# Performance work log

Hardware: AMD Instinct MI355X
Metric: run time of the kernel (lower is better)

Reference implementation:

```python
import jax, jax.numpy as jnp
import numpy as np

N_NODES = 100000
NEG_SLOPE = 0.01  # F.leaky_relu default


def _hetero_graphconv(x, src, dst, W, b, n_nodes):
    """HeteroGraphConv(aggregate='sum') of DGL GraphConv(norm='both') per edge type.

    x: [N, d_in]; src/dst: [R, E] int; W: [R, d_in, d_out]; b: [R, d_out].
    """
    n_rel = W.shape[0]
    ones = None
    out = jnp.zeros((n_nodes, W.shape[2]), dtype=x.dtype)
    for r in range(n_rel):  # small fixed number of relations
        s, d = src[r], dst[r]
        e_ones = jnp.ones(s.shape, dtype=x.dtype)
        deg_out = jnp.clip(jax.ops.segment_sum(e_ones, s, num_segments=n_nodes), 1.0)
        deg_in = jnp.clip(jax.ops.segment_sum(e_ones, d, num_segments=n_nodes), 1.0)
        # norm='both': scale src by out_deg^-1/2, aggregate, scale dst by in_deg^-1/2.
        # Apply weight before gather (aggregation is linear) to shrink edge traffic.
        h = (x * (deg_out ** -0.5)[:, None]) @ W[r]          # [N, d_out]
        agg = jax.ops.segment_sum(h[s], d, num_segments=n_nodes)  # gather-scatter over edges
        out = out + agg * (deg_in ** -0.5)[:, None] + b[r]
    return out


def setup_inputs() -> dict:
    key = jax.random.key(0)
    ks = jax.random.split(key, 8)
    d_in, d_h, d_out, n_cls, n_rel, n_edges = 256, 128, 128, 16, 3, 600000
    x = jax.random.normal(ks[0], (N_NODES, d_in), dtype=jnp.float32)
    src = jax.random.randint(ks[1], (n_rel, n_edges), 0, N_NODES, dtype=jnp.int32)
    dst = jax.random.randint(ks[2], (n_rel, n_edges), 0, N_NODES, dtype=jnp.int32)
    W0 = jax.random.normal(ks[3], (n_rel, d_in, d_h), dtype=jnp.float32) * (d_in ** -0.5)
    b0 = jnp.zeros((n_rel, d_h), dtype=jnp.float32)
    W1 = jax.random.normal(ks[4], (n_rel, d_h, d_out), dtype=jnp.float32) * (d_h ** -0.5)
    b1 = jnp.zeros((n_rel, d_out), dtype=jnp.float32)
    fc_W = jax.random.normal(ks[5], (d_out, n_cls), dtype=jnp.float32) * (d_out ** -0.5)
    fc_b = jnp.zeros((n_cls,), dtype=jnp.float32)
    return {"x": x, "src": src, "dst": dst, "W0": W0, "b0": b0,
            "W1": W1, "b1": b1, "fc_W": fc_W, "fc_b": fc_b}


def reference(x, src, dst, W0, b0, W1, b1, fc_W, fc_b):
    n = x.shape[0]
    h = _hetero_graphconv(x, src, dst, W0, b0, n)
    h = jax.nn.leaky_relu(h, negative_slope=NEG_SLOPE)  # dropout rate 0 (eval)
    h = _hetero_graphconv(h, src, dst, W1, b1, n)       # last layer: no activation
    logits = h @ fc_W + fc_b
    return (h, logits)
```

## Files before the change

### kernel.cpp

```cpp
#include <hip/hip_runtime.h>
#include <hip/hip_bf16.h>
#include <stdint.h>


typedef __attribute__((ext_vector_type(8))) short bf16x8;
typedef __attribute__((ext_vector_type(4))) float f32x4;
typedef unsigned short u16;

#define CUR_PAD 16
#define BF_K 8
#define CAP 32

__global__ __launch_bounds__(256)
void gemm0_bucket(const float* __restrict__ A,
                  const u16* __restrict__ Whi_all, const u16* __restrict__ Wlo_all,
                  u16* __restrict__ Cout_all, int M, int K, int Nn,
                  const int* __restrict__ src, const int* __restrict__ dst,
                  int* __restrict__ cnt_out, int* __restrict__ cursor,
                  int* __restrict__ bkt, int E, int N) {
    __shared__ u16 As_hi[128][40];
    __shared__ u16 As_lo[128][40];
    __shared__ u16 Bs_hi[128][40];
    __shared__ u16 Bs_lo[128][40];

    const int role = blockIdx.x;

    if (role >= 3) {
        const int r = role - 3;
        const int nbk = (E + 256 * BF_K - 1) / (256 * BF_K);
        const int b = blockIdx.y;
        if (b >= nbk) return;
        int e0 = b * (256 * BF_K) + threadIdx.x;
        int s[BF_K], d[BF_K], pos[BF_K];
#pragma unroll
        for (int j = 0; j < BF_K; j++) {
            int e = e0 + j * 256;
            bool v = e < E;
            s[j] = v ? src[(size_t)r * E + e] : -1;
            d[j] = v ? dst[(size_t)r * E + e] : 0;
        }
#pragma unroll
        for (int j = 0; j < BF_K; j++)
            if (s[j] >= 0)
                atomicAdd(cnt_out + ((size_t)s[j] * 3 + r) * CUR_PAD, 1);
#pragma unroll
        for (int j = 0; j < BF_K; j++)
            pos[j] = (s[j] >= 0)
                   ? atomicAdd(cursor + ((size_t)d[j] * 3 + r) * CUR_PAD, 1) : 0;
#pragma unroll
        for (int j = 0; j < BF_K; j++)
            if (s[j] >= 0 && pos[j] < CAP)
                bkt[((size_t)d[j] * 3 + r) * CAP + pos[j]] = r * N + s[j];
        return;
    }

    const int r = role;
    const u16* Whi = Whi_all + (size_t)r * K * 128;
    const u16* Wlo = Wlo_all + (size_t)r * K * 128;
    u16* Cout = Cout_all + (size_t)r * Nn * 128;

    const int tid  = threadIdx.x;
    const int m0   = blockIdx.y * 128;
    const int lane = tid & 63;
    const int wave = tid >> 6;
    const int wm   = (wave & 1) * 64;
    const int wn   = (wave >> 1) * 64;
    const int lm   = lane & 15;
    const int kq   = (lane >> 4) * 8;

    f32x4 acc[4][4];
#pragma unroll
    for (int i = 0; i < 4; i++)
#pragma unroll
        for (int j = 0; j < 4; j++) acc[i][j] = (f32x4){0.f, 0.f, 0.f, 0.f};

    const int srow = tid >> 1;
    const int skb  = (tid & 1) * 16;

    const bool valid = (m0 + srow) < M;
    const float* arow = A + (size_t)(m0 + srow) * K;
    const u16* whrow = Whi + (size_t)srow * K;
    const u16* wlrow = Wlo + (size_t)srow * K;

    for (int k0 = 0; k0 < K; k0 += 32) {
        float fa[16];
        if (valid) {
            *(float4*)&fa[0]  = *(const float4*)(arow + k0 + skb);
            *(float4*)&fa[4]  = *(const float4*)(arow + k0 + skb + 4);
            *(float4*)&fa[8]  = *(const float4*)(arow + k0 + skb + 8);
            *(float4*)&fa[12] = *(const float4*)(arow + k0 + skb + 12);
        } else {
#pragma unroll
            for (int i = 0; i < 16; i++) fa[i] = 0.f;
        }
        uint32_t ah[8], al[8];
#pragma unroll
        for (int p = 0; p < 8; p++) {
            float f0 = fa[2 * p], f1 = fa[2 * p + 1];
            uint32_t u0 = __float_as_uint(f0), u1 = __float_as_uint(f1);
            ah[p] = (u0 >> 16) | (u1 & 0xFFFF0000u);
            float l0 = f0 - __uint_as_float(u0 & 0xFFFF0000u);
            float l1 = f1 - __uint_as_float(u1 & 0xFFFF0000u);
            al[p] = (__float_as_uint(l0) >> 16) | (__float_as_uint(l1) & 0xFFFF0000u);
        }
        *(uint4*)&As_hi[srow][skb]     = *(uint4*)&ah[0];
        *(uint4*)&As_hi[srow][skb + 8] = *(uint4*)&ah[4];
        *(uint4*)&As_lo[srow][skb]     = *(uint4*)&al[0];
        *(uint4*)&As_lo[srow][skb + 8] = *(uint4*)&al[4];

        *(uint4*)&Bs_hi[srow][skb]     = *(const uint4*)(whrow + k0 + skb);
        *(uint4*)&Bs_hi[srow][skb + 8] = *(const uint4*)(whrow + k0 + skb + 8);
        *(uint4*)&Bs_lo[srow][skb]     = *(const uint4*)(wlrow + k0 + skb);
        *(uint4*)&Bs_lo[srow][skb + 8] = *(const uint4*)(wlrow + k0 + skb + 8);

        __syncthreads();

        bf16x8 a_hi[4], a_lo[4], b_hi[4], b_lo[4];
#pragma unroll
        for (int i = 0; i < 4; i++) {
            a_hi[i] = *(const bf16x8*)&As_hi[wm + i * 16 + lm][kq];
            a_lo[i] = *(const bf16x8*)&As_lo[wm + i * 16 + lm][kq];
            b_hi[i] = *(const bf16x8*)&Bs_hi[wn + i * 16 + lm][kq];
            b_lo[i] = *(const bf16x8*)&Bs_lo[wn + i * 16 + lm][kq];
        }
#pragma unroll
        for (int i = 0; i < 4; i++)
#pragma unroll
            for (int j = 0; j < 4; j++) {
                acc[i][j] = __builtin_amdgcn_mfma_f32_16x16x32_bf16(a_hi[i], b_hi[j], acc[i][j], 0, 0, 0);
                acc[i][j] = __builtin_amdgcn_mfma_f32_16x16x32_bf16(a_lo[i], b_hi[j], acc[i][j], 0, 0, 0);
                acc[i][j] = __builtin_amdgcn_mfma_f32_16x16x32_bf16(a_hi[i], b_lo[j], acc[i][j], 0, 0, 0);
            }
        __syncthreads();
    }

    const int rq = (lane >> 4) * 4;
#pragma unroll
    for (int i = 0; i < 4; i++) {
        int mbase = m0 + wm + i * 16 + rq;
#pragma unroll
        for (int j = 0; j < 4; j++) {
            int col = wn + j * 16 + lm;
#pragma unroll
            for (int rg = 0; rg < 4; rg++) {
                int m = mbase + rg;
                if (m < M) {
                    uint32_t u = __float_as_uint(acc[i][j][rg]);
                    Cout[(size_t)m * 128 + col] =
                        (u16)((u + 0x7FFFu + ((u >> 16) & 1u)) >> 16);
                }
            }
        }
    }
}

__global__ __launch_bounds__(256)
void reduce_scales_kernel(const int* __restrict__ cnt_out, const int* __restrict__ cursor,
                          float* __restrict__ s_out, float* __restrict__ s_in, int N) {
    int n = blockIdx.x * blockDim.x + threadIdx.x;
    if (n >= N) return;
#pragma unroll
    for (int r = 0; r < 3; r++) {
        int co = cnt_out[((size_t)n * 3 + r) * CUR_PAD];
        s_out[(size_t)r * N + n] = rsqrtf(fmaxf((float)co, 1.0f));
        int ci = cursor[((size_t)n * 3 + r) * CUR_PAD];
        s_in[(size_t)r * N + n] = rsqrtf(fmaxf((float)ci, 1.0f));
    }
}

__global__ __launch_bounds__(256)
void prep_w_kernel(const float* __restrict__ W0, const float* __restrict__ W1,
                   u16* __restrict__ w0hi, u16* __restrict__ w0lo,
                   u16* __restrict__ w1hi, u16* __restrict__ w1lo) {
    int idx = blockIdx.x * blockDim.x + threadIdx.x;
    const int n0 = 3 * 256 * 128;
    const int n1 = 3 * 128 * 128;
    if (idx >= n0 + n1) return;
    float f;
    u16 *phi, *plo;
    int oidx;
    if (idx < n0) {
        int r = idx / 32768, rem = idx % 32768;
        int n = rem / 256, k = rem % 256;
        f = W0[(size_t)r * 32768 + (size_t)k * 128 + n];
        phi = w0hi; plo = w0lo; oidx = idx;
    } else {
        int i2 = idx - n0;
        int r = i2 / 16384, rem = i2 % 16384;
        int n = rem / 128, k = rem % 128;
        f = W1[(size_t)r * 16384 + (size_t)k * 128 + n];
        phi = w1hi; plo = w1lo; oidx = i2;
    }
    uint32_t u = __float_as_uint(f);
    phi[oidx] = (u16)(u >> 16);
    float lo = f - __uint_as_float(u & 0xFFFF0000u);
    uint32_t ul = __float_as_uint(lo);
    plo[oidx] = (u16)((ul + 0x7FFFu + ((ul >> 16) & 1u)) >> 16);
}

__global__ __launch_bounds__(256)
void gemm_split_bf16(const float* __restrict__ A, const float* __restrict__ s_out,
                     const u16* __restrict__ Whi_all, const u16* __restrict__ Wlo_all,
                     u16* __restrict__ Cout_all, int M, int K, int Nn) {
    const int r = blockIdx.y;
    const float* scale = s_out + (size_t)r * Nn;
    const u16* Whi = Whi_all + (size_t)r * K * 128;
    const u16* Wlo = Wlo_all + (size_t)r * K * 128;
    u16* Cout = Cout_all + (size_t)r * Nn * 128;

    __shared__ u16 As_hi[128][40];
    __shared__ u16 As_lo[128][40];
    __shared__ u16 Bs_hi[128][40];
    __shared__ u16 Bs_lo[128][40];

    const int tid  = threadIdx.x;
    const int m0   = blockIdx.x * 128;
    const int lane = tid & 63;
    const int wave = tid >> 6;
    const int wm   = (wave & 1) * 64;
    const int wn   = (wave >> 1) * 64;
    const int lm   = lane & 15;
    const int kq   = (lane >> 4) * 8;

    f32x4 acc[4][4];
#pragma unroll
    for (int i = 0; i < 4; i++)
#pragma unroll
        for (int j = 0; j < 4; j++) acc[i][j] = (f32x4){0.f, 0.f, 0.f, 0.f};

    const int srow = tid >> 1;
    const int skb  = (tid & 1) * 16;

    const bool valid = (m0 + srow) < M;
    const float sval = valid ? scale[m0 + srow] : 0.f;
    const float* arow = A + (size_t)(m0 + srow) * K;
    const u16* whrow = Whi + (size_t)srow * K;
    const u16* wlrow = Wlo + (size_t)srow * K;

    for (int k0 = 0; k0 < K; k0 += 32) {
        float fa[16];
        if (valid) {
            *(float4*)&fa[0]  = *(const float4*)(arow + k0 + skb);
            *(float4*)&fa[4]  = *(const float4*)(arow + k0 + skb + 4);
            *(float4*)&fa[8]  = *(const float4*)(arow + k0 + skb + 8);
            *(float4*)&fa[12] = *(const float4*)(arow + k0 + skb + 12);
        } else {
#pragma unroll
            for (int i = 0; i < 16; i++) fa[i] = 0.f;
        }
        uint32_t ah[8], al[8];
#pragma unroll
        for (int p = 0; p < 8; p++) {
            float f0 = fa[2 * p] * sval, f1 = fa[2 * p + 1] * sval;
            uint32_t u0 = __float_as_uint(f0), u1 = __float_as_uint(f1);
            ah[p] = (u0 >> 16) | (u1 & 0xFFFF0000u);
            float l0 = f0 - __uint_as_float(u0 & 0xFFFF0000u);
            float l1 = f1 - __uint_as_float(u1 & 0xFFFF0000u);
            al[p] = (__float_as_uint(l0) >> 16) | (__float_as_uint(l1) & 0xFFFF0000u);
        }
        *(uint4*)&As_hi[srow][skb]     = *(uint4*)&ah[0];
        *(uint4*)&As_hi[srow][skb + 8] = *(uint4*)&ah[4];
        *(uint4*)&As_lo[srow][skb]     = *(uint4*)&al[0];
        *(uint4*)&As_lo[srow][skb + 8] = *(uint4*)&al[4];

        *(uint4*)&Bs_hi[srow][skb]     = *(const uint4*)(whrow + k0 + skb);
        *(uint4*)&Bs_hi[srow][skb + 8] = *(const uint4*)(whrow + k0 + skb + 8);
        *(uint4*)&Bs_lo[srow][skb]     = *(const uint4*)(wlrow + k0 + skb);
        *(uint4*)&Bs_lo[srow][skb + 8] = *(const uint4*)(wlrow + k0 + skb + 8);

        __syncthreads();

        bf16x8 a_hi[4], a_lo[4], b_hi[4], b_lo[4];
#pragma unroll
        for (int i = 0; i < 4; i++) {
            a_hi[i] = *(const bf16x8*)&As_hi[wm + i * 16 + lm][kq];
            a_lo[i] = *(const bf16x8*)&As_lo[wm + i * 16 + lm][kq];
            b_hi[i] = *(const bf16x8*)&Bs_hi[wn + i * 16 + lm][kq];
            b_lo[i] = *(const bf16x8*)&Bs_lo[wn + i * 16 + lm][kq];
        }
#pragma unroll
        for (int i = 0; i < 4; i++)
#pragma unroll
            for (int j = 0; j < 4; j++) {
                acc[i][j] = __builtin_amdgcn_mfma_f32_16x16x32_bf16(a_hi[i], b_hi[j], acc[i][j], 0, 0, 0);
                acc[i][j] = __builtin_amdgcn_mfma_f32_16x16x32_bf16(a_lo[i], b_hi[j], acc[i][j], 0, 0, 0);
                acc[i][j] = __builtin_amdgcn_mfma_f32_16x16x32_bf16(a_hi[i], b_lo[j], acc[i][j], 0, 0, 0);
            }
        __syncthreads();
    }

    const int rq = (lane >> 4) * 4;
#pragma unroll
    for (int i = 0; i < 4; i++) {
        int mbase = m0 + wm + i * 16 + rq;
#pragma unroll
        for (int j = 0; j < 4; j++) {
            int col = wn + j * 16 + lm;
#pragma unroll
            for (int rg = 0; rg < 4; rg++) {
                int m = mbase + rg;
                if (m < M) {
                    uint32_t u = __float_as_uint(acc[i][j][rg]);
                    Cout[(size_t)m * 128 + col] =
                        (u16)((u + 0x7FFFu + ((u >> 16) & 1u)) >> 16);
                }
            }
        }
    }
}

#define BF16_LO(u) __uint_as_float((u) << 16)
#define BF16_HI(u) __uint_as_float((u) & 0xFFFF0000u)

template<bool SOUT>
__device__ __forceinline__ void gather_all(const uint32_t* __restrict__ hb32,
                                           const int* __restrict__ cursor,
                                           const int* __restrict__ bkt,
                                           const float* __restrict__ s_in,
                                           const float* __restrict__ s_out,
                                           int node, int lane, int N,
                                           float& ox, float& oy) {
    const uint32_t* hrow = hb32 + lane;
    int d0 = __builtin_amdgcn_readfirstlane(cursor[(size_t)node * (3 * CUR_PAD)]);
    int d1 = __builtin_amdgcn_readfirstlane(cursor[(size_t)node * (3 * CUR_PAD) + CUR_PAD]);
    int d2 = __builtin_amdgcn_readfirstlane(cursor[(size_t)node * (3 * CUR_PAD) + 2 * CUR_PAD]);
    d0 = d0 > CAP ? CAP : d0;
    d1 = d1 > CAP ? CAP : d1;
    d2 = d2 > CAP ? CAP : d2;
    const int t01 = d0 + d1;
    const int tot = t01 + d2;
    const int* bp = bkt + (size_t)node * (3 * CAP);
    const float w0 = s_in[node];
    const float w1 = s_in[(size_t)N + node];
    const float w2 = s_in[(size_t)2 * N + node];
    float ax = 0.f, ay = 0.f, bx = 0.f, by = 0.f;
    float cx = 0.f, cy = 0.f, dx = 0.f, dy = 0.f;
    for (int j = 0; j < tot; j += 8) {
        uint32_t u[8];
        float w[8];
#pragma unroll
        for (int p = 0; p < 8; p++) {
            int jj = j + p;
            int r2 = (jj >= d0 ? 1 : 0) + (jj >= t01 ? 1 : 0);
            int off = r2 == 0 ? 0 : (r2 == 1 ? d0 - CAP : t01 - 2 * CAP);
            int bval = bp[jj - off];
            bool act = jj < tot;
            int idx = act ? bval : 0;
            float ws = r2 == 0 ? w0 : (r2 == 1 ? w1 : w2);
            if (SOUT) ws *= s_out[idx];
            w[p] = act ? ws : 0.f;
            u[p] = hrow[(size_t)idx * 64];
        }
#pragma unroll
        for (int p = 0; p < 8; p += 4) {
            ax = fmaf(BF16_LO(u[p]),     w[p],     ax);
            ay = fmaf(BF16_HI(u[p]),     w[p],     ay);
            bx = fmaf(BF16_LO(u[p + 1]), w[p + 1], bx);
            by = fmaf(BF16_HI(u[p + 1]), w[p + 1], by);
            cx = fmaf(BF16_LO(u[p + 2]), w[p + 2], cx);
            cy = fmaf(BF16_HI(u[p + 2]), w[p + 2], cy);
            dx = fmaf(BF16_LO(u[p + 3]), w[p + 3], dx);
            dy = fmaf(BF16_HI(u[p + 3]), w[p + 3], dy);
        }
    }
    ox = (ax + bx) + (cx + dx);
    oy = (ay + by) + (cy + dy);
}

__global__ __launch_bounds__(256)
void gather_l0(const u16* __restrict__ hb, const int* __restrict__ cursor,
               const int* __restrict__ bkt, const float* __restrict__ s_in,
               const float* __restrict__ s_out,
               const float* __restrict__ b, float* __restrict__ out, int N) {
    int node = blockIdx.x * 4 + (threadIdx.x >> 6);
    if (node >= N) return;
    int lane = threadIdx.x & 63;
    float tx, ty;
    gather_all<true>((const uint32_t*)hb, cursor, bkt, s_in, s_out, node, lane, N, tx, ty);
    int c0 = lane * 2;
    tx += b[c0] + b[128 + c0] + b[256 + c0];
    ty += b[c0 + 1] + b[128 + c0 + 1] + b[256 + c0 + 1];
    tx = fmaxf(tx, 0.f) + 0.01f * fminf(tx, 0.f);
    ty = fmaxf(ty, 0.f) + 0.01f * fminf(ty, 0.f);
    *(float2*)(out + (size_t)node * 128 + c0) = make_float2(tx, ty);
}

__global__ __launch_bounds__(256)
void gather_l1(const u16* __restrict__ hb, const int* __restrict__ cursor,
               const int* __restrict__ bkt, const float* __restrict__ s_in,
               const float* __restrict__ b, const float* __restrict__ fcW,
               const float* __restrict__ fcb, float* __restrict__ out_h,
               float* __restrict__ out_logits, int N) {
    int node = blockIdx.x * 4 + (threadIdx.x >> 6);
    if (node >= N) return;
    int lane = threadIdx.x & 63;
    float tx, ty;
    gather_all<false>((const uint32_t*)hb, cursor, bkt, s_in, nullptr, node, lane, N, tx, ty);
    int c0 = lane * 2;
    tx += b[c0] + b[128 + c0] + b[256 + c0];
    ty += b[c0 + 1] + b[128 + c0 + 1] + b[256 + c0 + 1];
    *(float2*)(out_h + (size_t)node * 128 + c0) = make_float2(tx, ty);

    const float* fc0 = fcW + (size_t)c0 * 16;
    float p[16];
#pragma unroll
    for (int j = 0; j < 16; j++) p[j] = tx * fc0[j] + ty * fc0[16 + j];
#pragma unroll
    for (int off = 1; off < 64; off <<= 1) {
#pragma unroll
        for (int j = 0; j < 16; j++) p[j] += __shfl_xor(p[j], off);
    }
    if (lane == 0) {
        float* lp = out_logits + (size_t)node * 16;
        *(float4*)(lp + 0)  = make_float4(p[0] + fcb[0],  p[1] + fcb[1],  p[2] + fcb[2],  p[3] + fcb[3]);
        *(float4*)(lp + 4)  = make_float4(p[4] + fcb[4],  p[5] + fcb[5],  p[6] + fcb[6],  p[7] + fcb[7]);
        *(float4*)(lp + 8)  = make_float4(p[8] + fcb[8],  p[9] + fcb[9],  p[10] + fcb[10], p[11] + fcb[11]);
        *(float4*)(lp + 12) = make_float4(p[12] + fcb[12], p[13] + fcb[13], p[14] + fcb[14], p[15] + fcb[15]);
    }
}

extern "C" void kernel_launch(void* const* d_in, const int* in_sizes, int n_in,
                              void* d_out, int out_size, void* d_ws, size_t ws_size,
                              hipStream_t stream) {
    const float* x   = (const float*)d_in[0];
    const int*   src = (const int*)d_in[1];
    const int*   dst = (const int*)d_in[2];
    const float* W0  = (const float*)d_in[3];
    const float* b0  = (const float*)d_in[4];
    const float* W1  = (const float*)d_in[5];
    const float* b1  = (const float*)d_in[6];
    const float* fcW = (const float*)d_in[7];
    const float* fcb = (const float*)d_in[8];

    const int N = in_sizes[0] / 256;
    const int E = in_sizes[1] / 3;

    float* out_h      = (float*)d_out;
    float* out_logits = out_h + (size_t)N * 128;

    char* p = (char*)d_ws;
    auto alloc = [&](size_t bytes) -> char* {
        char* q = p;
        p += (bytes + 255) & ~(size_t)255;
        return q;
    };
    float* s_out     = (float*)alloc(3 * (size_t)N * 4);
    float* s_in      = (float*)alloc(3 * (size_t)N * 4);
    int*   cnt_out   = (int*)alloc(3 * (size_t)N * CUR_PAD * 4);
    int*   cursor    = (int*)alloc(3 * (size_t)N * CUR_PAD * 4);
    int*   bkt       = (int*)alloc(3 * (size_t)N * CAP * 4 + 1024);
    u16*   w0hi      = (u16*)alloc(3 * 256 * 128 * 2);
    u16*   w0lo      = (u16*)alloc(3 * 256 * 128 * 2);
    u16*   w1hi      = (u16*)alloc(3 * 128 * 128 * 2);
    u16*   w1lo      = (u16*)alloc(3 * 128 * 128 * 2);
    u16*   hb        = (u16*)alloc(3 * (size_t)N * 128 * 2);
    float* acc0      = (float*)alloc((size_t)N * 128 * 4);

    hipMemsetAsync(cnt_out, 0, 2 * 3 * (size_t)N * CUR_PAD * sizeof(int), stream);

    prep_w_kernel<<<(3 * 256 * 128 + 3 * 128 * 128 + 255) / 256, 256, 0, stream>>>(
        W0, W1, w0hi, w0lo, w1hi, w1lo);

    int gemm_blocks   = (N + 127) / 128;
    int gather_blocks = (N + 3) / 4;

    gemm0_bucket<<<dim3(6, gemm_blocks), 256, 0, stream>>>(
        x, w0hi, w0lo, hb, N, 256, N, src, dst, cnt_out, cursor, bkt, E, N);

    reduce_scales_kernel<<<(N + 255) / 256, 256, 0, stream>>>(
        cnt_out, cursor, s_out, s_in, N);

    gather_l0<<<gather_blocks, 256, 0, stream>>>(hb, cursor, bkt, s_in, s_out, b0, acc0, N);

    gemm_split_bf16<<<dim3(gemm_blocks, 3), 256, 0, stream>>>(
        acc0, s_out, w1hi, w1lo, hb, N, 128, N);
    gather_l1<<<gather_blocks, 256, 0, stream>>>(hb, cursor, bkt, s_in, b1, fcW, fcb,
                                                 out_h, out_logits, N);
}
```

Before: 695.2 us.

## Overlap layer-1 GEMM with layer-0 gather via chunked fused kernels

Splits the node range into three chunks and launches fused kernels in which one column of blocks runs the layer-1 split-bf16 GEMM on an already-gathered chunk while the other blocks gather the next chunk of layer 0. This is meant to hide the GEMM behind the memory-bound gather instead of running the two phases back to back. It also drops the 16-int padding on the out-degree counters, which shrinks the memset and the reduce reads but packs the atomics closer together. A second hb buffer is needed for the overlap, with a fallback to the old path when the workspace is too small.

```diff
diff --git a/kernel.cpp b/kernel.cpp
--- a/kernel.cpp
+++ b/kernel.cpp
@@ -42,7 +42,7 @@
 #pragma unroll
         for (int j = 0; j < BF_K; j++)
             if (s[j] >= 0)
-                atomicAdd(cnt_out + ((size_t)s[j] * 3 + r) * CUR_PAD, 1);
+                atomicAdd(cnt_out + (size_t)s[j] * 3 + r, 1);
 #pragma unroll
         for (int j = 0; j < BF_K; j++)
             pos[j] = (s[j] >= 0)
@@ -161,7 +161,7 @@
     if (n >= N) return;
 #pragma unroll
     for (int r = 0; r < 3; r++) {
-        int co = cnt_out[((size_t)n * 3 + r) * CUR_PAD];
+        int co = cnt_out[(size_t)n * 3 + r];
         s_out[(size_t)r * N + n] = rsqrtf(fmaxf((float)co, 1.0f));
         int ci = cursor[((size_t)n * 3 + r) * CUR_PAD];
         s_in[(size_t)r * N + n] = rsqrtf(fmaxf((float)ci, 1.0f));
@@ -371,9 +371,10 @@
 void gather_l0(const u16* __restrict__ hb, const int* __restrict__ cursor,
                const int* __restrict__ bkt, const float* __restrict__ s_in,
                const float* __restrict__ s_out,
-               const float* __restrict__ b, float* __restrict__ out, int N) {
-    int node = blockIdx.x * 4 + (threadIdx.x >> 6);
-    if (node >= N) return;
+               const float* __restrict__ b, float* __restrict__ out,
+               int node0, int node_end, int N) {
+    int node = node0 + blockIdx.x * 4 + (threadIdx.x >> 6);
+    if (node >= node_end) return;
     int lane = threadIdx.x & 63;
     float tx, ty;
     gather_all<true>((const uint32_t*)hb, cursor, bkt, s_in, s_out, node, lane, N, tx, ty);
@@ -383,6 +384,142 @@
     tx = fmaxf(tx, 0.f) + 0.01f * fminf(tx, 0.f);
     ty = fmaxf(ty, 0.f) + 0.01f * fminf(ty, 0.f);
     *(float2*)(out + (size_t)node * 128 + c0) = make_float2(tx, ty);
+}
+
+__global__ __launch_bounds__(256)
+void k_gemm1_gather0(float* acc0,
+                     const float* __restrict__ s_out,
+                     const u16* __restrict__ w1hi, const u16* __restrict__ w1lo,
+                     u16* __restrict__ hb1,
+                     int tile_off, int ntile3, int M, int Nn,
+                     const u16* __restrict__ hb0, const int* __restrict__ cursor,
+                     const int* __restrict__ bkt, const float* __restrict__ s_in,
+                     const float* __restrict__ b0,
+                     int node0, int node_end, int N) {
+    __shared__ u16 As_hi[128][40];
+    __shared__ u16 As_lo[128][40];
+    __shared__ u16 Bs_hi[128][40];
+    __shared__ u16 Bs_lo[128][40];
+
+    if (blockIdx.x != 0) {
+        int gidx = ((int)blockIdx.x - 1) + 11 * (int)blockIdx.y;
+        int node = node0 + gidx * 4 + ((int)threadIdx.x >> 6);
+        if (node >= node_end) return;
+        int lane = threadIdx.x & 63;
+        float tx, ty;
+        gather_all<true>((const uint32_t*)hb0, cursor, bkt, s_in, s_out, node, lane, N, tx, ty);
+        int c0 = lane * 2;
+        tx += b0[c0] + b0[128 + c0] + b0[256 + c0];
+        ty += b0[c0 + 1] + b0[128 + c0 + 1] + b0[256 + c0 + 1];
+        tx = fmaxf(tx, 0.f) + 0.01f * fminf(tx, 0.f);
+        ty = fmaxf(ty, 0.f) + 0.01f * fminf(ty, 0.f);
+        *(float2*)(acc0 + (size_t)node * 128 + c0) = make_float2(tx, ty);
+        return;
+    }
+
+    int y = blockIdx.y;
+    if (y >= ntile3) return;
+    const int r = y % 3;
+    const int K = 128;
+    const float* scale = s_out + (size_t)r * Nn;
+    const u16* Whi = w1hi + (size_t)r * K * 128;
+    const u16* Wlo = w1lo + (size_t)r * K * 128;
+    u16* Cout = hb1 + (size_t)r * Nn * 128;
+
+    const int tid  = threadIdx.x;
+    const int m0   = (tile_off + y / 3) * 128;
+    const int lane = tid & 63;
+    const int wave = tid >> 6;
+    const int wm   = (wave & 1) * 64;
+    const int wn   = (wave >> 1) * 64;
+    const int lm   = lane & 15;
+    const int kq   = (lane >> 4) * 8;
+
+    f32x4 acc[4][4];
+#pragma unroll
+    for (int i = 0; i < 4; i++)
+#pragma unroll
+        for (int j = 0; j < 4; j++) acc[i][j] = (f32x4){0.f, 0.f, 0.f, 0.f};
+
+    const int srow = tid >> 1;
+    const int skb  = (tid & 1) * 16;
+
+    const bool valid = (m0 + srow) < M;
+    const float sval = valid ? scale[m0 + srow] : 0.f;
+    const float* arow = acc0 + (size_t)(m0 + srow) * K;
+    const u16* whrow = Whi + (size_t)srow * K;
+    const u16* wlrow = Wlo + (size_t)srow * K;
+
+    for (int k0 = 0; k0 < K; k0 += 32) {
+        float fa[16];
+        if (valid) {
+            *(float4*)&fa[0]  = *(const float4*)(arow + k0 + skb);
+            *(float4*)&fa[4]  = *(const float4*)(arow + k0 + skb + 4);
+            *(float4*)&fa[8]  = *(const float4*)(arow + k0 + skb + 8);
+            *(float4*)&fa[12] = *(const float4*)(arow + k0 + skb + 12);
+        } else {
+#pragma unroll
+            for (int i = 0; i < 16; i++) fa[i] = 0.f;
+        }
+        uint32_t ah[8], al[8];
+#pragma unroll
+        for (int p = 0; p < 8; p++) {
+            float f0 = fa[2 * p] * sval, f1 = fa[2 * p + 1] * sval;
+            uint32_t u0 = __float_as_uint(f0), u1 = __float_as_uint(f1);
+            ah[p] = (u0 >> 16) | (u1 & 0xFFFF0000u);
+            float l0 = f0 - __uint_as_float(u0 & 0xFFFF0000u);
+            float l1 = f1 - __uint_as_float(u1 & 0xFFFF0000u);
+            al[p] = (__float_as_uint(l0) >> 16) | (__float_as_uint(l1) & 0xFFFF0000u);
+        }
+        *(uint4*)&As_hi[srow][skb]     = *(uint4*)&ah[0];
+        *(uint4*)&As_hi[srow][skb + 8] = *(uint4*)&ah[4];
+        *(uint4*)&As_lo[srow][skb]     = *(uint4*)&al[0];
+        *(uint4*)&As_lo[srow][skb + 8] = *(uint4*)&al[4];
+
+        *(uint4*)&Bs_hi[srow][skb]     = *(const uint4*)(whrow + k0 + skb);
+        *(uint4*)&Bs_hi[srow][skb + 8] = *(const uint4*)(whrow + k0 + skb + 8);
+        *(uint4*)&Bs_lo[srow][skb]     = *(const uint4*)(wlrow + k0 + skb);
+        *(uint4*)&Bs_lo[srow][skb + 8] = *(const uint4*)(wlrow + k0 + skb + 8);
+
+        __syncthreads();
+
+        bf16x8 a_hi[4], a_lo[4], b_hi[4], b_lo[4];
+#pragma unroll
+        for (int i = 0; i < 4; i++) {
+            a_hi[i] = *(const bf16x8*)&As_hi[wm + i * 16 + lm][kq];
+            a_lo[i] = *(const bf16x8*)&As_lo[wm + i * 16 + lm][kq];
+            b_hi[i] = *(const bf16x8*)&Bs_hi[wn + i * 16 + lm][kq];
+            b_lo[i] = *(const bf16x8*)&Bs_lo[wn + i * 16 + lm][kq];
+        }
+#pragma unroll
+        for (int i = 0; i < 4; i++)
+#pragma unroll
+            for (int j = 0; j < 4; j++) {
+                acc[i][j] = __builtin_amdgcn_mfma_f32_16x16x32_bf16(a_hi[i], b_hi[j], acc[i][j], 0, 0, 0);
+                acc[i][j] = __builtin_amdgcn_mfma_f32_16x16x32_bf16(a_lo[i], b_hi[j], acc[i][j], 0, 0, 0);
+                acc[i][j] = __builtin_amdgcn_mfma_f32_16x16x32_bf16(a_hi[i], b_lo[j], acc[i][j], 0, 0, 0);
+            }
+        __syncthreads();
+    }
+
+    const int rq = (lane >> 4) * 4;
+#pragma unroll
+    for (int i = 0; i < 4; i++) {
+        int mbase = m0 + wm + i * 16 + rq;
+#pragma unroll
+        for (int j = 0; j < 4; j++) {
+            int col = wn + j * 16 + lm;
+#pragma unroll
+            for (int rg = 0; rg < 4; rg++) {
+                int m = mbase + rg;
+                if (m < M) {
+                    uint32_t u = __float_as_uint(acc[i][j][rg]);
+                    Cout[(size_t)m * 128 + col] =
+                        (u16)((u + 0x7FFFu + ((u >> 16) & 1u)) >> 16);
+                }
+            }
+        }
+    }
 }
 
 __global__ __launch_bounds__(256)
@@ -446,34 +583,72 @@
     };
     float* s_out     = (float*)alloc(3 * (size_t)N * 4);
     float* s_in      = (float*)alloc(3 * (size_t)N * 4);
-    int*   cnt_out   = (int*)alloc(3 * (size_t)N * CUR_PAD * 4);
+    int*   cnt_out   = (int*)alloc(3 * (size_t)N * 4);
     int*   cursor    = (int*)alloc(3 * (size_t)N * CUR_PAD * 4);
     int*   bkt       = (int*)alloc(3 * (size_t)N * CAP * 4 + 1024);
     u16*   w0hi      = (u16*)alloc(3 * 256 * 128 * 2);
     u16*   w0lo      = (u16*)alloc(3 * 256 * 128 * 2);
     u16*   w1hi      = (u16*)alloc(3 * 128 * 128 * 2);
     u16*   w1lo      = (u16*)alloc(3 * 128 * 128 * 2);
-    u16*   hb        = (u16*)alloc(3 * (size_t)N * 128 * 2);
+    u16*   hb0       = (u16*)alloc(3 * (size_t)N * 128 * 2);
     float* acc0      = (float*)alloc((size_t)N * 128 * 4);
-
-    hipMemsetAsync(cnt_out, 0, 2 * 3 * (size_t)N * CUR_PAD * sizeof(int), stream);
+    u16*   hb1       = (u16*)alloc(3 * (size_t)N * 128 * 2);
+
+    const bool pipelined = ((size_t)(p - (char*)d_ws) <= ws_size);
+    if (!pipelined) hb1 = hb0;
+
+    hipMemsetAsync(cnt_out, 0,
+                   (size_t)((char*)cursor - (char*)cnt_out)
+                   + 3 * (size_t)N * CUR_PAD * sizeof(int), stream);
 
     prep_w_kernel<<<(3 * 256 * 128 + 3 * 128 * 128 + 255) / 256, 256, 0, stream>>>(
         W0, W1, w0hi, w0lo, w1hi, w1lo);
 
-    int gemm_blocks   = (N + 127) / 128;
+    const int T = (N + 127) / 128;
     int gather_blocks = (N + 3) / 4;
 
-    gemm0_bucket<<<dim3(6, gemm_blocks), 256, 0, stream>>>(
-        x, w0hi, w0lo, hb, N, 256, N, src, dst, cnt_out, cursor, bkt, E, N);
+    gemm0_bucket<<<dim3(6, T), 256, 0, stream>>>(
+        x, w0hi, w0lo, hb0, N, 256, N, src, dst, cnt_out, cursor, bkt, E, N);
 
     reduce_scales_kernel<<<(N + 255) / 256, 256, 0, stream>>>(
         cnt_out, cursor, s_out, s_in, N);
 
-    gather_l0<<<gather_blocks, 256, 0, stream>>>(hb, cursor, bkt, s_in, s_out, b0, acc0, N);
-
-    gemm_split_bf16<<<dim3(gemm_blocks, 3), 256, 0, stream>>>(
-        acc0, s_out, w1hi, w1lo, hb, N, 128, N);
-    gather_l1<<<gather_blocks, 256, 0, stream>>>(hb, cursor, bkt, s_in, b1, fcW, fcb,
+    if (pipelined) {
+        const int T1 = (T + 2) / 3;
+        const int T2 = (T1 * 2 <= T) ? T1 : (T - T1);
+        const int T3 = T - T1 - T2;
+        const int n1 = (T1 * 128 < N) ? T1 * 128 : N;
+        const int n2 = ((T1 + T2) * 128 < N) ? (T1 + T2) * 128 : N;
+
+        gather_l0<<<(n1 + 3) / 4, 256, 0, stream>>>(
+            hb0, cursor, bkt, s_in, s_out, b0, acc0, 0, n1, N);
+
+        {
+            int gb = (n2 - n1 + 3) / 4;
+            int yd = T1 * 3 > (gb + 10) / 11 ? T1 * 3 : (gb + 10) / 11;
+            k_gemm1_gather0<<<dim3(12, yd), 256, 0, stream>>>(
+                acc0, s_out, w1hi, w1lo, hb1, 0, T1 * 3, N, N,
+                hb0, cursor, bkt, s_in, b0, n1, n2, N);
+        }
+        {
+            int gb = (N - n2 + 3) / 4;
+            int yd = T2 * 3 > (gb + 10) / 11 ? T2 * 3 : (gb + 10) / 11;
+            k_gemm1_gather0<<<dim3(12, yd), 256, 0, stream>>>(
+                acc0, s_out, w1hi, w1lo, hb1, T1, T2 * 3, N, N,
+                hb0, cursor, bkt, s_in, b0, n2, N, N);
+        }
+        if (T3 > 0) {
+            gemm_split_bf16<<<dim3(T3, 3), 256, 0, stream>>>(
+                acc0 + (size_t)n2 * 128, s_out + n2, w1hi, w1lo,
+                hb1 + (size_t)n2 * 128, N - n2, 128, N);
+        }
+    } else {
+        gather_l0<<<gather_blocks, 256, 0, stream>>>(
+            hb0, cursor, bkt, s_in, s_out, b0, acc0, 0, N, N);
+        gemm_split_bf16<<<dim3(T, 3), 256, 0, stream>>>(
+            acc0, s_out, w1hi, w1lo, hb1, N, 128, N);
+    }
+
+    gather_l1<<<gather_blocks, 256, 0, stream>>>(hb1, cursor, bkt, s_in, b1, fcW, fcb,
                                                  out_h, out_logits, N);
 }
```

New measurement: 797.3 us. 14.7% more time.
